# Performance work log

Hardware: AMD Instinct MI355X
Metric: run time of the kernel (lower is better)

## Reference

```python
import jax, jax.numpy as jnp
import numpy as np
from jax import lax

GAMMA = 1.0
B = 10            # forced by qnn_arch[0]=10 via w1 @ x in feedforward
N_TRAIN = 8192    # kernel support set size


def setup_inputs() -> dict:
    key = jax.random.key(0)
    ks = jax.random.split(key, 20)
    x = jax.random.normal(ks[0], (B, 3, 250, 250), jnp.float32)
    # CNN params (He-ish scale)
    conv1_w = jax.random.normal(ks[1], (6, 3, 5, 5), jnp.float32) * 0.1
    conv1_b = jax.random.normal(ks[2], (6,), jnp.float32) * 0.01
    conv2_w = jax.random.normal(ks[3], (15, 6, 3, 3), jnp.float32) * 0.1
    conv2_b = jax.random.normal(ks[4], (15,), jnp.float32) * 0.01
    fc1_w = jax.random.normal(ks[5], (120, 55815), jnp.float32) * 0.004
    fc1_b = jax.random.normal(ks[6], (120,), jnp.float32) * 0.01
    fc2_w = jax.random.normal(ks[7], (84, 120), jnp.float32) * 0.09
    fc2_b = jax.random.normal(ks[8], (84,), jnp.float32) * 0.01
    fc3_w = jax.random.normal(ks[9], (1, 84), jnp.float32) * 0.1
    fc3_b = jax.random.normal(ks[10], (1,), jnp.float32) * 0.01
    # QNN weights (original uses plain randn)
    qnn_w1 = jax.random.normal(ks[11], (20, 10), jnp.float32)
    qnn_w2 = jax.random.normal(ks[12], (5, 20), jnp.float32)
    # Precomputed training states: tanh(w2 @ tanh(w1 @ f)) per random feature f
    feats = jax.random.normal(ks[13], (N_TRAIN, 10), jnp.float32)
    train_states = jnp.tanh(jnp.tanh(feats @ qnn_w1.T) @ qnn_w2.T)  # [N_TRAIN, 5]
    kcls_w = jax.random.normal(ks[14], (2, N_TRAIN), jnp.float32) * 0.01
    kcls_b = jax.random.normal(ks[15], (2,), jnp.float32) * 0.01
    return {
        'x': x,
        'conv1_w': conv1_w, 'conv1_b': conv1_b,
        'conv2_w': conv2_w, 'conv2_b': conv2_b,
        'fc1_w': fc1_w, 'fc1_b': fc1_b,
        'fc2_w': fc2_w, 'fc2_b': fc2_b,
        'fc3_w': fc3_w, 'fc3_b': fc3_b,
        'qnn_w1': qnn_w1, 'qnn_w2': qnn_w2,
        'train_states': train_states,
        'kcls_w': kcls_w, 'kcls_b': kcls_b,
    }


def _conv(h, w, b, stride, pad):
    out = lax.conv_general_dilated(
        h, w, (stride, stride), [(pad, pad), (pad, pad)],
        dimension_numbers=('NCHW', 'OIHW', 'NCHW'))
    return out + b[None, :, None, None]


def _maxpool_2s1(h):
    return lax.reduce_window(h, -jnp.inf, lax.max, (1, 1, 2, 2), (1, 1, 1, 1), 'VALID')


def reference(x, conv1_w, conv1_b, conv2_w, conv2_b, fc1_w, fc1_b,
              fc2_w, fc2_b, fc3_w, fc3_b, qnn_w1, qnn_w2,
              train_states, kcls_w, kcls_b):
    h = jax.nn.relu(_conv(x, conv1_w, conv1_b, 2, 1))   # [10,6,124,124]
    h = _maxpool_2s1(h)                                 # [10,6,123,123]
    h = jax.nn.relu(_conv(h, conv2_w, conv2_b, 2, 1))   # [10,15,62,62]
    h = _maxpool_2s1(h)                                 # [10,15,61,61]
    h = h.reshape(h.shape[0], -1)                       # [10,55815]
    h = jax.nn.relu(h @ fc1_w.T + fc1_b)                # [10,120]
    h = jax.nn.relu(h @ fc2_w.T + fc2_b)                # [10,84]
    h = h @ fc3_w.T + fc3_b                             # [10,1]
    # QNN feedforward: batch dim B=10 is consumed as the qnn input dim
    s = jnp.tanh(qnn_w1 @ h)                            # [20,1]
    s = jnp.tanh(qnn_w2 @ s)                            # [5,1]
    fs = s[:, 0]                                        # [5]
    # Batched RBF kernel against all train states (replaces the Python .item() loop)
    d2 = jnp.sum((fs[None, :] - train_states) ** 2, axis=-1)  # [N_TRAIN]
    K = jnp.exp(-GAMMA * d2)                            # [N_TRAIN]
    out = K[None, :] @ kcls_w.T + kcls_b                # [1,2]
    return out
```

## Files before the change

### kernel.cpp

```cpp
#include <hip/hip_runtime.h>


#define ACT_STRIDE 55816

__global__ __launch_bounds__(128) void convpool1_k(
    const float* __restrict__ x, const float* __restrict__ w,
    const float* __restrict__ bias, float* __restrict__ out ) {
    const int b   = blockIdx.x;
    const int py0 = blockIdx.y * 4;
    const int px0 = blockIdx.z * 31;
    const int iy0 = 2 * py0 - 1;
    const int ix0 = 2 * px0 - 1;

    __shared__ float sxe[3][13][34];
    __shared__ float sxo[3][13][34];
    __shared__ float so[6][5][32];

    const int tid = threadIdx.x;

    for (int j = tid; j < 3 * 13 * 67; j += 128) {
        int c  = j % 67;
        int r  = (j / 67) % 13;
        int ic = j / (67 * 13);
        int ix = ix0 + c, iy = iy0 + r;
        float v = 0.f;
        if ((unsigned)ix < 250u && (unsigned)iy < 250u)
            v = x[((size_t)(b * 3 + ic) * 250 + iy) * 250 + ix];
        if (c & 1) sxo[ic][r][c >> 1] = v;
        else       sxe[ic][r][c >> 1] = v;
    }
    __syncthreads();

    for (int p = tid; p < 5 * 32; p += 128) {
        int oxl = p & 31;
        int oyl = p >> 5;
        float acc[6];
        #pragma unroll
        for (int o = 0; o < 6; ++o) acc[o] = bias[o];
        #pragma unroll
        for (int ic = 0; ic < 3; ++ic) {
            #pragma unroll
            for (int ky = 0; ky < 5; ++ky) {
                int r = 2 * oyl + ky;
                #pragma unroll
                for (int kx = 0; kx < 5; ++kx) {
                    float xv = (kx & 1) ? sxo[ic][r][oxl + (kx >> 1)]
                                        : sxe[ic][r][oxl + (kx >> 1)];
                    #pragma unroll
                    for (int o = 0; o < 6; ++o)
                        acc[o] += w[((o * 3 + ic) * 5 + ky) * 5 + kx] * xv;
                }
            }
        }
        #pragma unroll
        for (int o = 0; o < 6; ++o) so[o][oyl][oxl] = fmaxf(acc[o], 0.f);
    }
    __syncthreads();

    for (int j = tid; j < 6 * 4 * 31; j += 128) {
        int pxl = j % 31;
        int pyl = (j / 31) & 3;
        int oc  = j / 124;
        int px = px0 + pxl, py = py0 + pyl;
        if (px < 123 && py < 123) {
            float v = fmaxf(fmaxf(so[oc][pyl][pxl],     so[oc][pyl][pxl + 1]),
                            fmaxf(so[oc][pyl + 1][pxl], so[oc][pyl + 1][pxl + 1]));
            out[((size_t)(b * 6 + oc) * 123 + py) * 123 + px] = v;
        }
    }
}

__global__ __launch_bounds__(128) void convpool2_k(
    const float* __restrict__ in , const float* __restrict__ w,
    const float* __restrict__ bias, float* __restrict__ out ) {
    const int b   = blockIdx.x;
    const int py0 = blockIdx.y * 2;
    const int px0 = blockIdx.z * 31;
    const int n_py = (61 - py0) < 2 ? (61 - py0) : 2;
    const int n_oy = n_py + 1;
    const int iy0 = 2 * py0 - 1;
    const int ix0 = 2 * px0 - 1;

    __shared__ float sx[6][7][68];
    __shared__ float so[15][3][32];

    const int tid = threadIdx.x;

    for (int j = tid; j < 6 * 7 * 65; j += 128) {
        int col = j % 65;
        int r   = (j / 65) % 7;
        int ic  = j / (65 * 7);
        int ix = ix0 + col, iy = iy0 + r;
        float v = 0.f;
        if ((unsigned)ix < 123u && (unsigned)iy < 123u)
            v = in[((size_t)(b * 6 + ic) * 123 + iy) * 123 + ix];
        sx[ic][r][col] = v;
    }
    __syncthreads();

    for (int p = tid; p < n_oy * 32; p += 128) {
        int oxl = p & 31;
        int oyl = p >> 5;
        if (px0 + oxl < 62) {
            float acc[15];
            #pragma unroll
            for (int o = 0; o < 15; ++o) acc[o] = bias[o];
            #pragma unroll
            for (int ic = 0; ic < 6; ++ic) {
                #pragma unroll
                for (int ky = 0; ky < 3; ++ky) {
                    const float* xr = &sx[ic][2 * oyl + ky][2 * oxl];
                    #pragma unroll
                    for (int kx = 0; kx < 3; ++kx) {
                        float xv = xr[kx];
                        #pragma unroll
                        for (int o = 0; o < 15; ++o)
                            acc[o] += w[((o * 6 + ic) * 3 + ky) * 3 + kx] * xv;
                    }
                }
            }
            #pragma unroll
            for (int o = 0; o < 15; ++o) so[o][oyl][oxl] = fmaxf(acc[o], 0.f);
        }
    }
    __syncthreads();

    for (int j = tid; j < 15 * 2 * 31; j += 128) {
        int pxl = j % 31;
        int pyl = (j / 31) & 1;
        int oc  = j / 62;
        int px = px0 + pxl, py = py0 + pyl;
        if (pyl < n_py && px < 61) {
            float v = fmaxf(fmaxf(so[oc][pyl][pxl],     so[oc][pyl][pxl + 1]),
                            fmaxf(so[oc][pyl + 1][pxl], so[oc][pyl + 1][pxl + 1]));
            out[(size_t)b * ACT_STRIDE + ((size_t)oc * 61 + py) * 61 + px] = v;
        }
    }
}

#define FC1_K      55815
#define FC1_CHUNK  768
#define FC1_NC     73
#define FC1_RT     15

__global__ __launch_bounds__(256) void fc1_partial_k(
    const float* __restrict__ act ,
    const float* __restrict__ w   ,
    float* __restrict__ partials  ) {
    int rt  = blockIdx.x;
    int c   = blockIdx.y;
    int tid = threadIdx.x;
    int wave = tid >> 6, lane = tid & 63;
    int k0 = c * FC1_CHUNK;
    int k1 = k0 + FC1_CHUNK; if (k1 > FC1_K) k1 = FC1_K;
    int r0 = rt * 8 + wave * 2;
    const float* w0 = w + (size_t)r0 * FC1_K;
    const float* w1 = w + (size_t)(r0 + 1) * FC1_K;

    float acc0[10], acc1[10];
    #pragma unroll
    for (int b = 0; b < 10; ++b) { acc0[b] = 0.f; acc1[b] = 0.f; }

    for (int k = k0 + lane * 4; k < k1; k += 256) {
        if (k + 4 <= k1) {
            float4 a4[10];
            #pragma unroll
            for (int b = 0; b < 10; ++b)
                a4[b] = *reinterpret_cast<const float4*>(act + (size_t)b * ACT_STRIDE + k);
            float w00 = w0[k], w01 = w0[k + 1], w02 = w0[k + 2], w03 = w0[k + 3];
            float w10 = w1[k], w11 = w1[k + 1], w12 = w1[k + 2], w13 = w1[k + 3];
            #pragma unroll
            for (int b = 0; b < 10; ++b) {
                acc0[b] += w00 * a4[b].x + w01 * a4[b].y + w02 * a4[b].z + w03 * a4[b].w;
                acc1[b] += w10 * a4[b].x + w11 * a4[b].y + w12 * a4[b].z + w13 * a4[b].w;
            }
        } else {
            for (int j = 0; j < k1 - k; ++j) {
                float wv0 = w0[k + j], wv1 = w1[k + j];
                #pragma unroll
                for (int b = 0; b < 10; ++b) {
                    float av = act[(size_t)b * ACT_STRIDE + k + j];
                    acc0[b] += wv0 * av;
                    acc1[b] += wv1 * av;
                }
            }
        }
    }
    #pragma unroll
    for (int b = 0; b < 10; ++b) {
        float v0 = acc0[b], v1 = acc1[b];
        for (int off = 32; off > 0; off >>= 1) {
            v0 += __shfl_down(v0, off);
            v1 += __shfl_down(v1, off);
        }
        if (lane == 0) {
            size_t base = ((size_t)c * 120 + r0) * 10;
            partials[base + b]      = v0;
            partials[base + 10 + b] = v1;
        }
    }
}

__global__ __launch_bounds__(128) void fcA_k(
    const float* __restrict__ part , const float* __restrict__ fc1_b,
    const float* __restrict__ fc2_w, const float* __restrict__ fc2_b,
    const float* __restrict__ fc3_w, const float* __restrict__ fc3_b,
    float* __restrict__ h3 ) {
    const int b = blockIdx.x;
    const int tid = threadIdx.x;
    __shared__ float s_act[120];
    __shared__ float s_fc2[84];

    if (tid < 120) {
        float s = 0.f;
        for (int c = 0; c < FC1_NC; ++c) s += part[((size_t)c * 120 + tid) * 10 + b];
        s_act[tid] = fmaxf(s + fc1_b[tid], 0.f);
    }
    __syncthreads();
    if (tid < 84) {
        float acc = fc2_b[tid];
        #pragma unroll 4
        for (int k = 0; k < 120; ++k) acc += s_act[k] * fc2_w[tid * 120 + k];
        s_fc2[tid] = fmaxf(acc, 0.f);
    }
    __syncthreads();
    if (tid < 64) {
        float v = s_fc2[tid] * fc3_w[tid];
        if (tid < 20) v += s_fc2[tid + 64] * fc3_w[tid + 64];
        for (int off = 32; off > 0; off >>= 1) v += __shfl_down(v, off);
        if (tid == 0) h3[b] = v + fc3_b[0];
    }
}

__global__ __launch_bounds__(128) void clsB_k(
    const float* __restrict__ h3 ,
    const float* __restrict__ qw1, const float* __restrict__ qw2,
    const float* __restrict__ ts , const float* __restrict__ kw ,
    float* __restrict__ partials ) {
    int tid = threadIdx.x;
    __shared__ float s_h3[10], s_s1[20], s_fs[5];
    if (tid < 10) s_h3[tid] = h3[tid];
    __syncthreads();
    if (tid < 20) {
        float acc = 0.f;
        for (int b = 0; b < 10; ++b) acc += qw1[tid * 10 + b] * s_h3[b];
        s_s1[tid] = tanhf(acc);
    }
    __syncthreads();
    if (tid < 5) {
        float acc = 0.f;
        for (int j = 0; j < 20; ++j) acc += qw2[tid * 20 + j] * s_s1[j];
        s_fs[tid] = tanhf(acc);
    }
    __syncthreads();

    float f0 = s_fs[0], f1 = s_fs[1], f2 = s_fs[2], f3 = s_fs[3], f4 = s_fs[4];
    int n = blockIdx.x * 128 + tid;
    const float* t = ts + (size_t)n * 5;
    float d0 = f0 - t[0], d1 = f1 - t[1], d2 = f2 - t[2], d3 = f3 - t[3], d4 = f4 - t[4];
    float Kv = expf(-(d0 * d0 + d1 * d1 + d2 * d2 + d3 * d3 + d4 * d4));
    float a0 = Kv * kw[n];
    float a1 = Kv * kw[8192 + n];
    for (int off = 32; off > 0; off >>= 1) {
        a0 += __shfl_down(a0, off);
        a1 += __shfl_down(a1, off);
    }
    __shared__ float l0[2], l1[2];
    int wave = tid >> 6, lane = tid & 63;
    if (lane == 0) { l0[wave] = a0; l1[wave] = a1; }
    __syncthreads();
    if (tid == 0) {
        partials[blockIdx.x * 2 + 0] = l0[0] + l0[1];
        partials[blockIdx.x * 2 + 1] = l1[0] + l1[1];
    }
}

__global__ void clsC_k(const float* __restrict__ partials,
                       const float* __restrict__ kb, float* __restrict__ out) {
    int c = threadIdx.x;
    if (c < 2) {
        float acc = kb[c];
        for (int i = 0; i < 64; ++i) acc += partials[i * 2 + c];
        out[c] = acc;
    }
}

extern "C" void kernel_launch(void* const* d_in, const int* in_sizes, int n_in,
                              void* d_out, int out_size, void* d_ws, size_t ws_size,
                              hipStream_t stream) {
    const float* x        = (const float*)d_in[0];
    const float* conv1_w  = (const float*)d_in[1];
    const float* conv1_b  = (const float*)d_in[2];
    const float* conv2_w  = (const float*)d_in[3];
    const float* conv2_b  = (const float*)d_in[4];
    const float* fc1_w    = (const float*)d_in[5];
    const float* fc1_b    = (const float*)d_in[6];
    const float* fc2_w    = (const float*)d_in[7];
    const float* fc2_b    = (const float*)d_in[8];
    const float* fc3_w    = (const float*)d_in[9];
    const float* fc3_b    = (const float*)d_in[10];
    const float* qnn_w1   = (const float*)d_in[11];
    const float* qnn_w2   = (const float*)d_in[12];
    const float* tstates  = (const float*)d_in[13];
    const float* kcls_w   = (const float*)d_in[14];
    const float* kcls_b   = (const float*)d_in[15];

    float* ws = (float*)d_ws;
    float* p1       = ws;
    float* p2       = p1 + 907740;
    float* fc1_part = p2 + 558160;
    float* h3       = fc1_part + 87600;
    float* partials = h3 + 16;

    convpool1_k<<<dim3(10, 31, 4), 128, 0, stream>>>(x, conv1_w, conv1_b, p1);
    convpool2_k<<<dim3(10, 31, 2), 128, 0, stream>>>(p1, conv2_w, conv2_b, p2);
    fc1_partial_k<<<dim3(FC1_RT, FC1_NC), 256, 0, stream>>>(p2, fc1_w, fc1_part);
    fcA_k<<<10, 128, 0, stream>>>(fc1_part, fc1_b, fc2_w, fc2_b, fc3_w, fc3_b, h3);
    clsB_k<<<64, 128, 0, stream>>>(h3, qnn_w1, qnn_w2, tstates, kcls_w, partials);
    clsC_k<<<1, 64, 0, stream>>>(partials, kcls_b, (float*)d_out);
}
```

Before: 90.31 us.

## Compute 2x2 conv outputs per thread and fuse maxpool into registers

```diff
diff --git a/kernel.cpp b/kernel.cpp
--- a/kernel.cpp
+++ b/kernel.cpp
@@ -3,69 +3,75 @@
 
 #define ACT_STRIDE 55816
 
-__global__ __launch_bounds__(128) void convpool1_k(
+__global__ __launch_bounds__(256) void convpool1_k(
     const float* __restrict__ x, const float* __restrict__ w,
     const float* __restrict__ bias, float* __restrict__ out ) {
     const int b   = blockIdx.x;
     const int py0 = blockIdx.y * 4;
-    const int px0 = blockIdx.z * 31;
+    const int px0 = blockIdx.z * 64;
     const int iy0 = 2 * py0 - 1;
     const int ix0 = 2 * px0 - 1;
 
-    __shared__ float sxe[3][13][34];
-    __shared__ float sxo[3][13][34];
-    __shared__ float so[6][5][32];
+    __shared__ float sx[3][13][136];
 
     const int tid = threadIdx.x;
 
-    for (int j = tid; j < 3 * 13 * 67; j += 128) {
-        int c  = j % 67;
-        int r  = (j / 67) % 13;
-        int ic = j / (67 * 13);
+    for (int j = tid; j < 3 * 13 * 133; j += 256) {
+        int c  = j % 133;
+        int r  = (j / 133) % 13;
+        int ic = j / (133 * 13);
         int ix = ix0 + c, iy = iy0 + r;
         float v = 0.f;
         if ((unsigned)ix < 250u && (unsigned)iy < 250u)
             v = x[((size_t)(b * 3 + ic) * 250 + iy) * 250 + ix];
-        if (c & 1) sxo[ic][r][c >> 1] = v;
-        else       sxe[ic][r][c >> 1] = v;
-    }
-    __syncthreads();
-
-    for (int p = tid; p < 5 * 32; p += 128) {
-        int oxl = p & 31;
-        int oyl = p >> 5;
-        float acc[6];
+        sx[ic][r][c] = v;
+    }
+    __syncthreads();
+
+    const int pxl = tid & 63;
+    const int pyl = tid >> 6;
+    const int py = py0 + pyl, px = px0 + pxl;
+
+    float acc[6][4];
+    #pragma unroll
+    for (int o = 0; o < 6; ++o) {
+        float bv = bias[o];
         #pragma unroll
-        for (int o = 0; o < 6; ++o) acc[o] = bias[o];
+        for (int q = 0; q < 4; ++q) acc[o][q] = bv;
+    }
+
+    #pragma unroll
+    for (int ic = 0; ic < 3; ++ic) {
         #pragma unroll
-        for (int ic = 0; ic < 3; ++ic) {
-            #pragma unroll
-            for (int ky = 0; ky < 5; ++ky) {
-                int r = 2 * oyl + ky;
+        for (int r = 0; r < 7; ++r) {
+            #pragma unroll
+            for (int c = 0; c < 7; ++c) {
+                float xv = sx[ic][2 * pyl + r][2 * pxl + c];
                 #pragma unroll
-                for (int kx = 0; kx < 5; ++kx) {
-                    float xv = (kx & 1) ? sxo[ic][r][oxl + (kx >> 1)]
-                                        : sxe[ic][r][oxl + (kx >> 1)];
+                for (int dy = 0; dy < 2; ++dy) {
+                    int ky = r - 2 * dy;
+                    if (ky < 0 || ky >= 5) continue;
                     #pragma unroll
-                    for (int o = 0; o < 6; ++o)
-                        acc[o] += w[((o * 3 + ic) * 5 + ky) * 5 + kx] * xv;
+                    for (int dx = 0; dx < 2; ++dx) {
+                        int kx = c - 2 * dx;
+                        if (kx < 0 || kx >= 5) continue;
+                        #pragma unroll
+                        for (int o = 0; o < 6; ++o)
+                            acc[o][dy * 2 + dx] =
+                                fmaf(w[((o * 3 + ic) * 5 + ky) * 5 + kx], xv,
+                                     acc[o][dy * 2 + dx]);
+                    }
                 }
             }
         }
+    }
+
+    if (py < 123 && px < 123) {
         #pragma unroll
-        for (int o = 0; o < 6; ++o) so[o][oyl][oxl] = fmaxf(acc[o], 0.f);
-    }
-    __syncthreads();
-
-    for (int j = tid; j < 6 * 4 * 31; j += 128) {
-        int pxl = j % 31;
-        int pyl = (j / 31) & 3;
-        int oc  = j / 124;
-        int px = px0 + pxl, py = py0 + pyl;
-        if (px < 123 && py < 123) {
-            float v = fmaxf(fmaxf(so[oc][pyl][pxl],     so[oc][pyl][pxl + 1]),
-                            fmaxf(so[oc][pyl + 1][pxl], so[oc][pyl + 1][pxl + 1]));
-            out[((size_t)(b * 6 + oc) * 123 + py) * 123 + px] = v;
+        for (int o = 0; o < 6; ++o) {
+            float m = fmaxf(fmaxf(acc[o][0], acc[o][1]),
+                            fmaxf(acc[o][2], acc[o][3]));
+            out[((size_t)(b * 6 + o) * 123 + py) * 123 + px] = fmaxf(m, 0.f);
         }
     }
 }
@@ -312,7 +318,7 @@
     float* h3       = fc1_part + 87600;
     float* partials = h3 + 16;
 
-    convpool1_k<<<dim3(10, 31, 4), 128, 0, stream>>>(x, conv1_w, conv1_b, p1);
+    convpool1_k<<<dim3(10, 31, 2), 256, 0, stream>>>(x, conv1_w, conv1_b, p1);
     convpool2_k<<<dim3(10, 31, 2), 128, 0, stream>>>(p1, conv2_w, conv2_b, p2);
     fc1_partial_k<<<dim3(FC1_RT, FC1_NC), 256, 0, stream>>>(p2, fc1_w, fc1_part);
     fcA_k<<<10, 128, 0, stream>>>(fc1_part, fc1_b, fc2_w, fc2_b, fc3_w, fc3_b, h3);
```

Measured after the change: 91.52 us. About the same (+1.3%).
